# Performance work log

Measured on AMD Instinct MI355X. Metric: run time of the kernel, lower is better.

Reference implementation:

```python
import jax, jax.numpy as jnp
import numpy as np

# TT config (matches init_kwargs)
NUM_TABLES = 4
P = (100, 100, 100)          # tt_p_shapes, prod = num_embeddings = 1e6
Q = (4, 4, 4)                # tt_q_shapes, prod = embedding_dim = 64
R = (1, 32, 32, 1)           # tt_ranks with boundary ranks
BAGS_PER_TABLE = 8192
POOL = 16                    # indices per bag


def setup_inputs() -> dict:
    key = jax.random.key(0)
    k1, k2, k3, k4 = jax.random.split(key, 4)
    nnz = NUM_TABLES * BAGS_PER_TABLE * POOL      # 524288
    B = NUM_TABLES * BAGS_PER_TABLE               # 32768 bags total
    indices = jax.random.randint(k1, (nnz,), 0, P[0] * P[1] * P[2], dtype=jnp.int64)
    offsets = (jnp.arange(B + 1, dtype=jnp.int64) * POOL)
    scale = 0.05  # small init, akin to approx-normal weight_dist
    tt_core_0 = jax.random.normal(k2, (NUM_TABLES, P[0], R[0] * Q[0] * R[1]), dtype=jnp.float32) * scale
    tt_core_1 = jax.random.normal(k3, (NUM_TABLES, P[1], R[1] * Q[1] * R[2]), dtype=jnp.float32) * scale
    tt_core_2 = jax.random.normal(k4, (NUM_TABLES, P[2], R[2] * Q[2] * R[3]), dtype=jnp.float32) * scale
    return {"indices": indices, "offsets": offsets,
            "tt_core_0": tt_core_0, "tt_core_1": tt_core_1, "tt_core_2": tt_core_2}


def reference(indices, offsets, tt_core_0, tt_core_1, tt_core_2):
    nnz = indices.shape[0]
    B = offsets.shape[0] - 1
    bags_per_table = B // NUM_TABLES

    # bag id for each nonzero (embedding-bag semantics), then table id per nonzero
    rowidx = jnp.searchsorted(offsets, jnp.arange(nnz, dtype=offsets.dtype), side='right') - 1
    tableidx = rowidx // bags_per_table

    # decompose flat row index into TT indices (C-order over p-shapes,
    # matching tt_matrix_to_full row layout)
    i0 = indices // (P[1] * P[2])
    i1 = (indices // P[2]) % P[1]
    i2 = indices % P[2]

    # gather per-lookup core slices
    c0 = tt_core_0[tableidx, i0].reshape(nnz, Q[0], R[1])          # r0 == 1
    c1 = tt_core_1[tableidx, i1].reshape(nnz, R[1], Q[1], R[2])
    c2 = tt_core_2[tableidx, i2].reshape(nnz, R[2], Q[2])          # r3 == 1

    # on-the-fly TT contraction to reconstruct embedding rows [nnz, D]
    t = jnp.einsum('nar,nrbs->nabs', c0, c1)                       # [nnz, q0, q1, r2]
    rows = jnp.einsum('nabs,nsc->nabc', t, c2).reshape(nnz, Q[0] * Q[1] * Q[2])

    # sum-pool per bag
    out = jax.ops.segment_sum(rows, rowidx, num_segments=B)        # [B, D]
    return out
```

## Files before the change

kernel.cpp:

```cpp
#include <hip/hip_runtime.h>
#include <stdint.h>

#define NT 4
#define PP 100
#define TT_BYTES (4ull * 100 * 100 * 1024)


typedef __attribute__((ext_vector_type(8))) short short8;
typedef __attribute__((ext_vector_type(4))) float floatx4;
union U4S8 { uint4 u; short8 s; };

__device__ __forceinline__ uint32_t f2bf(float f) {
    union { float f; uint32_t u; } v; v.f = f;
    uint32_t u = v.u;
    return (u + 0x7fffu + ((u >> 16) & 1u)) >> 16;
}

__global__ __launch_bounds__(128, 3)
void tt_phase1(const float* __restrict__ c0g, const float* __restrict__ c1g,
               const float* __restrict__ c2g, unsigned short* __restrict__ tT,
               uint32_t* __restrict__ c2a) {
    __shared__ float c1s[32 * 128];
    __shared__ float c0t[16 * 136];

    int blk = blockIdx.x;
    int tid = threadIdx.x;

    if (blk < 200) {
        int t = blk * 128 + tid;
        int jp = t & 3, sgrp = (t >> 2) & 3, nn = (t >> 4) & 3, rest = t >> 6;
        int i2 = rest % PP, tb = rest / PP;
        const float* src = c2g + (size_t)(tb * PP + i2) * 128;
        int s = sgrp * 8 + 2 * jp;
        c2a[t] = f2bf(src[s * 4 + nn]) | (f2bf(src[(s + 1) * 4 + nn]) << 16);
    }

    int tab   = blk / 700;
    int rem   = blk % 700;
    int i1    = rem / 7;
    int chunk = rem % 7;
    int i0_base = chunk * 16;

    const float4* c1p = (const float4*)(c1g + (size_t)(tab * PP + i1) * 4096);
    float4* c1v = (float4*)c1s;
    #pragma unroll
    for (int it = 0; it < 8; ++it) c1v[tid + 128 * it] = c1p[tid + 128 * it];

    #pragma unroll
    for (int it = 0; it < 16; ++it) {
        int f = tid + 128 * it;
        int i0l = f >> 7;
        int x   = f & 127;
        int a = x >> 5, r = x & 31;
        int i0 = i0_base + i0l; if (i0 > PP - 1) i0 = PP - 1;
        c0t[i0l * 136 + r * 4 + a] = c0g[(size_t)(tab * PP + i0) * 128 + x];
    }
    __syncthreads();

    int u  = tid >> 4;
    int sg = tid & 15;

    float acc[2][2][16];
    #pragma unroll
    for (int ii = 0; ii < 2; ++ii)
        #pragma unroll
        for (int e = 0; e < 2; ++e)
            #pragma unroll
            for (int q = 0; q < 16; ++q) acc[ii][e][q] = 0.f;

    #pragma unroll 4
    for (int r = 0; r < 32; ++r) {
        float4 av0 = *(const float4*)&c0t[(2 * u) * 136 + r * 4];
        float4 av1 = *(const float4*)&c0t[(2 * u + 1) * 136 + r * 4];
        const float* a0 = (const float*)&av0;
        const float* a1 = (const float*)&av1;
        #pragma unroll
        for (int b = 0; b < 4; ++b) {
            float2 bv = *(const float2*)&c1s[r * 128 + b * 32 + 2 * sg];
            #pragma unroll
            for (int a = 0; a < 4; ++a) {
                acc[0][0][a * 4 + b] += a0[a] * bv.x;
                acc[0][1][a * 4 + b] += a0[a] * bv.y;
                acc[1][0][a * 4 + b] += a1[a] * bv.x;
                acc[1][1][a * 4 + b] += a1[a] * bv.y;
            }
        }
    }

    #pragma unroll
    for (int ii = 0; ii < 2; ++ii) {
        int i0 = i0_base + 2 * u + ii;
        if (i0 >= PP) continue;
        size_t combo = (size_t)tab * 10000 + (size_t)i0 * 100 + (size_t)i1;
        uint32_t* bp = (uint32_t*)((char*)tT + combo * 1024) + sg;
        #pragma unroll
        for (int ab = 0; ab < 16; ++ab)
            bp[ab * 16] = f2bf(acc[ii][0][ab]) | (f2bf(acc[ii][1][ab]) << 16);
    }
}

__global__ __launch_bounds__(256, 3)
void tt_phase2(const int* __restrict__ indices, const int* __restrict__ offsets,
               const unsigned short* __restrict__ tT, const uint32_t* __restrict__ c2a,
               float* __restrict__ out, int bags_per_table, int B) {
    __shared__ float obuf[4][64];
    int lane = threadIdx.x & 63;
    int wv   = threadIdx.x >> 6;
    int blk  = blockIdx.x;

    int tab, bag;
    if (((gridDim.x & 7) == 0) && ((B & 31) == 0)) {
        int xcd = blk & 7;
        tab = xcd >> 1;
        int within = ((blk >> 3) << 1) + (xcd & 1);
        bag = tab * bags_per_table + within * 4 + wv;
    } else {
        bag = blk * 4 + wv;
        tab = bag / bags_per_table;
    }
    if (bag >= B) return;

    int n = lane & 15, quad = lane >> 4;
    int aoff = n * 64 + quad * 16;
    int boff = (n & 3) * 64 + quad * 16;

    int start = __builtin_amdgcn_readfirstlane(offsets[bag]);

    const char* tbase = (const char*)tT + (size_t)tab * 10000u * 1024u;
    const char* cbase = (const char*)c2a + (size_t)tab * PP * 256u;

    uint4 af[16], bf[16];
    #pragma unroll
    for (int j = 0; j < 16; ++j) {
        uint32_t idx = (uint32_t)__builtin_amdgcn_readfirstlane(indices[start + j]);
        uint32_t i0 = idx / 10000u;
        uint32_t r1 = idx - i0 * 10000u;
        uint32_t i1 = r1 / 100u;
        uint32_t i2 = r1 - i1 * 100u;
        uint32_t combo = i0 * 100u + i1;
        af[j] = *(const uint4*)(tbase + (size_t)combo * 1024u + aoff);
        bf[j] = *(const uint4*)(cbase + (size_t)i2 * 256u + boff);
    }
    __builtin_amdgcn_sched_barrier(0);

    floatx4 acc0 = {0.f, 0.f, 0.f, 0.f};
    floatx4 acc1 = {0.f, 0.f, 0.f, 0.f};
    #pragma unroll
    for (int j = 0; j < 16; j += 2) {
        U4S8 a0, b0, a1, b1;
        a0.u = af[j];     b0.u = bf[j];
        a1.u = af[j + 1]; b1.u = bf[j + 1];
        acc0 = __builtin_amdgcn_mfma_f32_16x16x32_bf16(a0.s, b0.s, acc0, 0, 0, 0);
        acc1 = __builtin_amdgcn_mfma_f32_16x16x32_bf16(a1.s, b1.s, acc1, 0, 0, 0);
    }

    if (n < 4) {
        #pragma unroll
        for (int r = 0; r < 4; ++r)
            obuf[wv][quad * 16 + r * 4 + n] = acc0[r] + acc1[r];
    }
    __asm__ volatile("s_waitcnt lgkmcnt(0)" ::: "memory");
    if (lane < 16) {
        float4 v = *(const float4*)&obuf[wv][lane * 4];
        ((float4*)(out + (size_t)bag * 64))[lane] = v;
    }
}

extern "C" void kernel_launch(void* const* d_in, const int* in_sizes, int n_in,
                              void* d_out, int out_size, void* d_ws, size_t ws_size,
                              hipStream_t stream) {
    const int*   indices = (const int*)d_in[0];
    const int*   offsets = (const int*)d_in[1];
    const float* c0      = (const float*)d_in[2];
    const float* c1      = (const float*)d_in[3];
    const float* c2      = (const float*)d_in[4];
    float* out = (float*)d_out;

    int B = in_sizes[1] - 1;
    int bags_per_table = B / NT;

    unsigned short* tT  = (unsigned short*)d_ws;
    uint32_t*       c2a = (uint32_t*)((char*)d_ws + TT_BYTES);

    tt_phase1<<<dim3(NT * PP * 7), dim3(128), 0, stream>>>(c0, c1, c2, tT, c2a);
    tt_phase2<<<dim3((B + 3) / 4), dim3(256), 0, stream>>>(indices, offsets, tT, c2a, out,
                                                           bags_per_table, B);
}
```

Before: 166.6 us.

## Stage TT slabs via global_load_lds and cache c2 table in LDS for phase2

Phase2 now loads each lookup's 1 KB core-product slab straight into LDS with global_load_lds, in two batches of 8 per wave, instead of holding 16 uint4 register fragments. The block also copies the whole per-table c2 array (25.6 KB) into shared memory and reads B fragments from there. Indices are read as int4 vectors, and the XCD-aware bag remapping and the launch-bounds occupancy hints are removed. This cuts register pressure and scattered global B loads, at the cost of about 58 KB of LDS per block, which limits occupancy. It also adds a per-block c2 copy and serialises the two load batches.

After: 168.8 us. About the same (+1.3%).

```diff
diff --git a/kernel.cpp b/kernel.cpp
--- a/kernel.cpp
+++ b/kernel.cpp
@@ -9,6 +9,10 @@
 typedef __attribute__((ext_vector_type(8))) short short8;
 typedef __attribute__((ext_vector_type(4))) float floatx4;
 union U4S8 { uint4 u; short8 s; };
+
+#define GLOAD_LDS16(g, l) __builtin_amdgcn_global_load_lds(                  \
+    (const __attribute__((address_space(1))) void*)(g),                      \
+    (__attribute__((address_space(3))) void*)(l), 16, 0, 0)
 
 __device__ __forceinline__ uint32_t f2bf(float f) {
     union { float f; uint32_t u; } v; v.f = f;
@@ -16,7 +20,7 @@
     return (u + 0x7fffu + ((u >> 16) & 1u)) >> 16;
 }
 
-__global__ __launch_bounds__(128, 3)
+__global__ __launch_bounds__(128)
 void tt_phase1(const float* __restrict__ c0g, const float* __restrict__ c1g,
                const float* __restrict__ c2g, unsigned short* __restrict__ tT,
                uint32_t* __restrict__ c2a) {
@@ -99,65 +103,86 @@
     }
 }
 
-__global__ __launch_bounds__(256, 3)
+__global__ __launch_bounds__(256)
 void tt_phase2(const int* __restrict__ indices, const int* __restrict__ offsets,
                const unsigned short* __restrict__ tT, const uint32_t* __restrict__ c2a,
                float* __restrict__ out, int bags_per_table, int B) {
+    __shared__ uint4 c2s[1600];
+    __shared__ char  aslab[4][8192];
     __shared__ float obuf[4][64];
-    int lane = threadIdx.x & 63;
-    int wv   = threadIdx.x >> 6;
-    int blk  = blockIdx.x;
-
-    int tab, bag;
-    if (((gridDim.x & 7) == 0) && ((B & 31) == 0)) {
-        int xcd = blk & 7;
-        tab = xcd >> 1;
-        int within = ((blk >> 3) << 1) + (xcd & 1);
-        bag = tab * bags_per_table + within * 4 + wv;
-    } else {
-        bag = blk * 4 + wv;
-        tab = bag / bags_per_table;
-    }
+
+    int tid  = threadIdx.x;
+    int lane = tid & 63, wv = tid >> 6;
+    int bag  = blockIdx.x * 4 + wv;
     if (bag >= B) return;
+    int tab  = (int)(((long)blockIdx.x * 4) / bags_per_table);
+
+    const uint4* csrc = (const uint4*)c2a + (size_t)tab * 1600;
+    #pragma unroll
+    for (int it = 0; it < 7; ++it) {
+        int i = tid + 256 * it;
+        if (i < 1600) c2s[i] = csrc[i];
+    }
+
+    int start = offsets[bag];
+    uint32_t code[16];
+    {
+        const int4* ip = (const int4*)&indices[start];
+        int4 v0 = ip[0], v1 = ip[1], v2 = ip[2], v3 = ip[3];
+        int raw[16] = { v0.x, v0.y, v0.z, v0.w, v1.x, v1.y, v1.z, v1.w,
+                        v2.x, v2.y, v2.z, v2.w, v3.x, v3.y, v3.z, v3.w };
+        #pragma unroll
+        for (int j = 0; j < 16; ++j) {
+            uint32_t idx = (uint32_t)raw[j];
+            uint32_t i0 = idx / 10000u;
+            uint32_t r1 = idx - i0 * 10000u;
+            uint32_t i1 = r1 / 100u;
+            uint32_t i2 = r1 - i1 * 100u;
+            code[j] = (i0 * 100u + i1) * 128u + i2;
+        }
+    }
+
+    const char* tbl = (const char*)tT + (size_t)tab * 10000u * 1024u
+                                      + (size_t)lane * 16u;
+
+    #pragma unroll
+    for (int j = 0; j < 8; ++j)
+        GLOAD_LDS16(tbl + (size_t)(code[j] >> 7) * 1024u, &aslab[wv][j * 1024]);
+
+    __syncthreads();
 
     int n = lane & 15, quad = lane >> 4;
     int aoff = n * 64 + quad * 16;
-    int boff = (n & 3) * 64 + quad * 16;
-
-    int start = __builtin_amdgcn_readfirstlane(offsets[bag]);
-
-    const char* tbase = (const char*)tT + (size_t)tab * 10000u * 1024u;
-    const char* cbase = (const char*)c2a + (size_t)tab * PP * 256u;
-
-    uint4 af[16], bf[16];
-    #pragma unroll
-    for (int j = 0; j < 16; ++j) {
-        uint32_t idx = (uint32_t)__builtin_amdgcn_readfirstlane(indices[start + j]);
-        uint32_t i0 = idx / 10000u;
-        uint32_t r1 = idx - i0 * 10000u;
-        uint32_t i1 = r1 / 100u;
-        uint32_t i2 = r1 - i1 * 100u;
-        uint32_t combo = i0 * 100u + i1;
-        af[j] = *(const uint4*)(tbase + (size_t)combo * 1024u + aoff);
-        bf[j] = *(const uint4*)(cbase + (size_t)i2 * 256u + boff);
-    }
-    __builtin_amdgcn_sched_barrier(0);
-
-    floatx4 acc0 = {0.f, 0.f, 0.f, 0.f};
-    floatx4 acc1 = {0.f, 0.f, 0.f, 0.f};
-    #pragma unroll
-    for (int j = 0; j < 16; j += 2) {
-        U4S8 a0, b0, a1, b1;
-        a0.u = af[j];     b0.u = bf[j];
-        a1.u = af[j + 1]; b1.u = bf[j + 1];
-        acc0 = __builtin_amdgcn_mfma_f32_16x16x32_bf16(a0.s, b0.s, acc0, 0, 0, 0);
-        acc1 = __builtin_amdgcn_mfma_f32_16x16x32_bf16(a1.s, b1.s, acc1, 0, 0, 0);
+    int boff = (n & 3) * 4 + quad;
+
+    floatx4 acc = {0.f, 0.f, 0.f, 0.f};
+    #pragma unroll
+    for (int j = 0; j < 8; ++j) {
+        U4S8 a, b;
+        a.u = *(const uint4*)&aslab[wv][j * 1024 + aoff];
+        b.u = c2s[(code[j] & 127u) * 16u + boff];
+        acc = __builtin_amdgcn_mfma_f32_16x16x32_bf16(a.s, b.s, acc, 0, 0, 0);
+    }
+
+    __asm__ volatile("s_waitcnt lgkmcnt(0)" ::: "memory");
+
+    #pragma unroll
+    for (int j = 8; j < 16; ++j)
+        GLOAD_LDS16(tbl + (size_t)(code[j] >> 7) * 1024u, &aslab[wv][(j - 8) * 1024]);
+    __asm__ volatile("s_waitcnt vmcnt(0)" ::: "memory");
+
+    #pragma unroll
+    for (int j = 8; j < 16; ++j) {
+        U4S8 a, b;
+        a.u = *(const uint4*)&aslab[wv][(j - 8) * 1024 + aoff];
+        b.u = c2s[(code[j] & 127u) * 16u + boff];
+        acc = __builtin_amdgcn_mfma_f32_16x16x32_bf16(a.s, b.s, acc, 0, 0, 0);
     }
 
     if (n < 4) {
         #pragma unroll
         for (int r = 0; r < 4; ++r)
-            obuf[wv][quad * 16 + r * 4 + n] = acc0[r] + acc1[r];
+            obuf[wv][quad * 16 + r * 4 + n] = acc[r];
     }
     __asm__ volatile("s_waitcnt lgkmcnt(0)" ::: "memory");
     if (lane < 16) {
```
